# Kernel optimization log

Hardware: AMD Instinct MI355X
Metric: run time of the kernel (lower is better)

The kernel has to match this reference:

```python
import jax, jax.numpy as jnp
import numpy as np

N_HEADS = 32
N_KV_HEADS = 8
HEAD_DIM = 64
D_MODEL = 2048
SLIDING_WINDOW = 512
ROPE_THETA = 10000.0
PAST_LENGTH = 0
EPS = 1e-6


def setup_inputs() -> dict:
    key = jax.random.key(0)
    k1, k2, k3 = jax.random.split(key, 3)
    B, S = 1, 2048
    q_size = N_HEADS * HEAD_DIM
    kv_size = N_KV_HEADS * HEAD_DIM
    return {
        "x": jax.random.normal(k1, (B, S, D_MODEL), dtype=jnp.float32),
        "w_qkv": jax.random.normal(k2, (q_size + 2 * kv_size, D_MODEL), dtype=jnp.float32) * (D_MODEL ** -0.5),
        "w_out": jax.random.normal(k3, (D_MODEL, q_size), dtype=jnp.float32) * (q_size ** -0.5),
        "q_norm_w": jnp.ones((HEAD_DIM,), dtype=jnp.float32),
        "k_norm_w": jnp.ones((HEAD_DIM,), dtype=jnp.float32),
    }


def _rms_norm(x, w):
    xf = x.astype(jnp.float32)
    rms = jax.lax.rsqrt(jnp.mean(xf * xf, axis=-1, keepdims=True) + EPS)
    return (xf * rms).astype(x.dtype) * w


def _rope(q, k, past_length):
    # q: [b, h, s, d], k: [b, kv, s, d]
    s, d = q.shape[2], q.shape[3]
    inv_freq = 1.0 / (ROPE_THETA ** (jnp.arange(0, d, 2, dtype=jnp.float32) / d))
    pos = jnp.arange(s, dtype=jnp.float32) + past_length
    ang = pos[:, None] * inv_freq[None, :]            # [s, d/2]
    emb = jnp.concatenate([ang, ang], axis=-1)        # [s, d]
    cos, sin = jnp.cos(emb), jnp.sin(emb)

    def rot_half(x):
        x1, x2 = jnp.split(x, 2, axis=-1)
        return jnp.concatenate([-x2, x1], axis=-1)

    q = q * cos + rot_half(q) * sin
    k = k * cos + rot_half(k) * sin
    return q, k


def _sliding_mask(seq_len, total_len, past_length):
    q_idx = jnp.arange(seq_len)[:, None]
    k_idx = jnp.arange(total_len)[None, :]
    causal = (q_idx + past_length) >= k_idx
    window = (q_idx + past_length - k_idx) < SLIDING_WINDOW
    keep = causal & window
    return jnp.where(keep, 0.0, -jnp.inf).astype(jnp.float32)[None, None]


def reference(x, w_qkv, w_out, q_norm_w, k_norm_w):
    b, s, _ = x.shape
    n_rep = N_HEADS // N_KV_HEADS
    q_size = N_HEADS * HEAD_DIM
    kv_size = N_KV_HEADS * HEAD_DIM

    qkv = jnp.einsum('bsd,od->bso', x, w_qkv)
    q, k, v = jnp.split(qkv, [q_size, q_size + kv_size], axis=-1)
    q = q.reshape(b, s, N_HEADS, HEAD_DIM).transpose(0, 2, 1, 3)
    k = k.reshape(b, s, N_KV_HEADS, HEAD_DIM).transpose(0, 2, 1, 3)
    v = v.reshape(b, s, N_KV_HEADS, HEAD_DIM).transpose(0, 2, 1, 3)

    q = _rms_norm(q, q_norm_w)
    k = _rms_norm(k, k_norm_w)
    q, k = _rope(q, k, PAST_LENGTH)

    k_rep = jnp.repeat(k, n_rep, axis=1)  # [b, H, s, d]
    v_rep = jnp.repeat(v, n_rep, axis=1)

    scale = HEAD_DIM ** -0.5
    scores = jnp.einsum('bhqd,bhkd->bhqk', q, k_rep) * scale
    scores = scores + _sliding_mask(s, s, PAST_LENGTH)
    probs = jax.nn.softmax(scores, axis=-1)
    attn = jnp.einsum('bhqk,bhkd->bhqd', probs, v_rep)

    attn = attn.transpose(0, 2, 1, 3).reshape(b, s, q_size)
    return jnp.einsum('bso,do->bsd', attn, w_out)
```

## Files before the change

kernel.cpp:

```cpp
#include <hip/hip_runtime.h>

typedef unsigned short u16;
typedef unsigned int u32;
typedef __bf16 bf16x8 __attribute__((ext_vector_type(8)));
typedef float f32x4 __attribute__((ext_vector_type(4)));
typedef float f32x16 __attribute__((ext_vector_type(16)));
typedef u16 u16x8 __attribute__((ext_vector_type(8)));
typedef u32 u32x2 __attribute__((ext_vector_type(2)));
typedef u32 u32x4 __attribute__((ext_vector_type(4)));

#define MFMA16(a, b, c) __builtin_amdgcn_mfma_f32_16x16x32_bf16((a), (b), (c), 0, 0, 0)
#define MFMA32(a, b, c) __builtin_amdgcn_mfma_f32_32x32x16_bf16((a), (b), (c), 0, 0, 0)

__device__ __forceinline__ u16 f2bf(float f) {
    unsigned int u = __float_as_uint(f);
    u = (u + 0x7FFF + ((u >> 16) & 1)) >> 16;
    return (u16)u;
}

__device__ __forceinline__ u32 cvtpk(float a, float b) {
    u32 d;
    asm("v_cvt_pk_bf16_f32 %0, %1, %2" : "=v"(d) : "v"(a), "v"(b));
    return d;
}

__device__ __forceinline__ void gld_lds16(const u16* g, u16* l) {
    __builtin_amdgcn_global_load_lds(
        (const __attribute__((address_space(1))) unsigned int*)g,
        (__attribute__((address_space(3))) unsigned int*)l, 16, 0, 0);
}

__global__ __launch_bounds__(256) void cvt_bf16(const float* __restrict__ in,
                                                u16* __restrict__ out, int n4) {
    int idx = blockIdx.x * blockDim.x + threadIdx.x;
    int stride = gridDim.x * blockDim.x;
    for (int i = idx; i < n4; i += stride) {
        float4 v = reinterpret_cast<const float4*>(in)[i];
        ushort4 o;
        o.x = f2bf(v.x); o.y = f2bf(v.y); o.z = f2bf(v.z); o.w = f2bf(v.w);
        reinterpret_cast<ushort4*>(out)[i] = o;
    }
}

__global__ __launch_bounds__(256) void reduce_add(const float4* __restrict__ a,
                                                  const float4* __restrict__ b,
                                                  float4* __restrict__ o, int n4) {
    int idx = blockIdx.x * blockDim.x + threadIdx.x;
    int stride = gridDim.x * blockDim.x;
    for (int i = idx; i < n4; i += stride) {
        float4 va = a[i], vb = b[i];
        float4 vo = {va.x + vb.x, va.y + vb.y, va.z + vb.z, va.w + vb.w};
        o[i] = vo;
    }
}

template <int SPLITK>
__global__ __launch_bounds__(256) void gemm_bt(const u16* __restrict__ A,
                                               const u16* __restrict__ B,
                                               float* __restrict__ C,
                                               int M, int N, int K) {
    __shared__ __align__(16) u16 As[3][128 * 32];
    __shared__ __align__(16) u16 Bs[3][128 * 32];

    int nbn = N >> 7;
    int bid = blockIdx.x;
    int nwg = (M >> 7) * nbn;
    int cpx = nwg >> 3;
    int wg = (bid & 7) * cpx + (bid >> 3);
    int tm = wg / nbn, tn = wg % nbn;
    int m0 = tm << 7, n0 = tn << 7;

    int Ks = K / SPLITK;
    int kbase = blockIdx.y * Ks;
    float* Cs = C + (size_t)blockIdx.y * ((size_t)M * N);

    int t = threadIdx.x;
    int w = t >> 6, l = t & 63, lrow = l & 15, lhi = l >> 4;
    int wr = w >> 1, wc = w & 1;

    int e0 = t * 8;
    int row0 = t >> 2;
    int col0 = (((t & 3) ^ ((t >> 3) & 3)) << 3);

    const u16* Ag = A + (size_t)m0 * K + kbase;
    const u16* Bg = B + (size_t)n0 * K + kbase;

    auto stage = [&](int sbuf, int kt) {
        int k0 = kt << 5;
        gld_lds16(Ag + (size_t)row0 * K + k0 + col0, &As[sbuf][e0]);
        gld_lds16(Ag + (size_t)(row0 + 64) * K + k0 + col0, &As[sbuf][e0 + 2048]);
        gld_lds16(Bg + (size_t)row0 * K + k0 + col0, &Bs[sbuf][e0]);
        gld_lds16(Bg + (size_t)(row0 + 64) * K + k0 + col0, &Bs[sbuf][e0 + 2048]);
    };

    f32x4 acc[4][4] = {};
    int NT = Ks >> 5;
    stage(0, 0); stage(1, 1); stage(2, 2);
    asm volatile("s_waitcnt vmcnt(8)" ::: "memory");
    asm volatile("s_barrier" ::: "memory");
    int cur = 0;
    for (int kt = 0; kt < NT; ++kt) {
        bf16x8 af[4], bfr[4];
#pragma unroll
        for (int i = 0; i < 4; ++i) {
            int row = wr * 64 + i * 16 + lrow;
            af[i] = *(const bf16x8*)&As[cur][row * 32 + ((lhi ^ ((row >> 1) & 3)) << 3)];
        }
#pragma unroll
        for (int j = 0; j < 4; ++j) {
            int row = wc * 64 + j * 16 + lrow;
            bfr[j] = *(const bf16x8*)&Bs[cur][row * 32 + ((lhi ^ ((row >> 1) & 3)) << 3)];
        }
        asm volatile("s_waitcnt lgkmcnt(0)" ::: "memory");
        __builtin_amdgcn_sched_barrier(0);
        asm volatile("s_barrier" ::: "memory");
        if (kt + 3 < NT) stage(cur, kt + 3);
#pragma unroll
        for (int i = 0; i < 4; ++i)
#pragma unroll
            for (int j = 0; j < 4; ++j)
                acc[i][j] = MFMA16(af[i], bfr[j], acc[i][j]);
        if (kt + 1 < NT) {
            if (kt + 3 < NT)      asm volatile("s_waitcnt vmcnt(8)" ::: "memory");
            else if (kt + 2 < NT) asm volatile("s_waitcnt vmcnt(4)" ::: "memory");
            else                  asm volatile("s_waitcnt vmcnt(0)" ::: "memory");
            asm volatile("s_barrier" ::: "memory");
        }
        cur = (cur == 2) ? 0 : cur + 1;
    }
#pragma unroll
    for (int i = 0; i < 4; ++i) {
#pragma unroll
        for (int j = 0; j < 4; ++j) {
            int crow = m0 + wr * 64 + i * 16 + lhi * 4;
            int ccol = n0 + wc * 64 + j * 16 + lrow;
            float* cp = Cs + (size_t)crow * N + ccol;
#pragma unroll
            for (int r2 = 0; r2 < 4; ++r2) cp[(size_t)r2 * N] = acc[i][j][r2];
        }
    }
}

__global__ __launch_bounds__(256) void qkv_post(const float* __restrict__ qkv0,
                                                const float* __restrict__ qkv1,
                                                const float* __restrict__ qw,
                                                const float* __restrict__ kw,
                                                u16* __restrict__ qb,
                                                u16* __restrict__ kb,
                                                u16* __restrict__ vb) {
    const float C = 0.18033688011112042f;
    int s = blockIdx.x;
    int t = threadIdx.x, w = t >> 6, lane = t & 63;
    const float* row0 = qkv0 + (size_t)s * 3072;
    const float* row1 = qkv1 + (size_t)s * 3072;
    int d2 = lane & 31;
    float inv = exp2f(-(float)d2 * (13.287712379549449f / 32.0f));
    float ang = (float)s * inv;
    float cs = cosf(ang), sn = sinf(ang);
    for (int h = w; h < 48; h += 4) {
        float v = row0[h * 64 + lane] + row1[h * 64 + lane];
        if (h < 40) {
            float ss = v * v;
#pragma unroll
            for (int m = 32; m; m >>= 1) ss += __shfl_xor(ss, m);
            float rms = rsqrtf(ss * (1.0f / 64.0f) + 1e-6f);
            float wgt = (h < 32) ? qw[lane] : kw[lane];
            v = v * rms * wgt;
            float part = __shfl_xor(v, 32);
            float rot = (lane < 32) ? -part : part;
            v = v * cs + rot * sn;
            if (h < 32)
                qb[((size_t)h * 2048 + s) * 64 + lane] = f2bf(v * C);
            else
                kb[((size_t)(h - 32) * 2048 + s) * 64 + lane] = f2bf(v);
        } else {
            vb[((size_t)(h - 40) * 2048 + s) * 64 + lane] = f2bf(v);
        }
    }
}

__global__ __launch_bounds__(256) void transpose_v(const u16* __restrict__ vb,
                                                   u16* __restrict__ vt) {
    int kv = blockIdx.y;
    int s0 = blockIdx.x * 256;
    __shared__ __align__(16) u16 tile[64][256];
    int t = threadIdx.x;
    int sl = t >> 3;
    int d0 = (t & 7) * 8;
#pragma unroll
    for (int j = 0; j < 8; ++j) {
        int s = sl + j * 32;
        u16x8 v = *(const u16x8*)(vb + ((size_t)kv * 2048 + s0 + s) * 64 + d0);
#pragma unroll
        for (int e = 0; e < 8; ++e) tile[d0 + e][s] = v[e];
    }
    __syncthreads();
    int d = t >> 2;
    int so = (t & 3) * 64;
#pragma unroll
    for (int j = 0; j < 8; ++j) {
        int s_local = so + j * 8;
        *(u16x8*)(vt + ((size_t)kv * 64 + d) * 2048 + s0 + s_local) =
            *(const u16x8*)&tile[d][s_local];
    }
}

__global__ __launch_bounds__(256) void attn_fa7(const u16* __restrict__ qb,
                                                const u16* __restrict__ kb,
                                                const u16* __restrict__ vt,
                                                u16* __restrict__ ab) {
    int qt = blockIdx.x, h = blockIdx.y, kv = h >> 2;
    int t = threadIdx.x, w = t >> 6, l = t & 63;
    int lq = l & 31, hi = l >> 5;
    int qlo_blk = qt * 128;
    int qlo = qlo_blk + w * 32;
    __shared__ __align__(16) u16 Kt[2][32 * 64];
    __shared__ __align__(16) u16 Vt[2][64 * 32];
    __shared__ u16 sm[4][32][66];

    const u16* qrow = qb + ((size_t)h * 2048 + qlo + lq) * 64 + hi * 8;
    bf16x8 qf[4];
#pragma unroll
    for (int dk = 0; dk < 4; ++dk) qf[dk] = *(const bf16x8*)(qrow + dk * 16);

    f32x16 oa = {}, ob = {};
    float lsum = 0.f;

    int ktA = (qlo_blk >= 512) ? ((qlo_blk >> 5) - 16) : 0;
    int ktB = (qlo_blk >> 5) + 3;
    const u16* kb_h = kb + (size_t)kv * 2048 * 64;
    const u16* vt_h = vt + (size_t)kv * 64 * 2048;

    int sk_row = t >> 3, sk_c = ((t & 7) ^ (sk_row & 7)) << 3;
    int sv_row = t >> 2, sv_c = (((t & 3) ^ ((t >> 3) & 3))) << 3;

    auto stage = [&](int buf, int kt) {
        int k0 = kt << 5;
        gld_lds16(kb_h + (size_t)(k0 + sk_row) * 64 + sk_c, &Kt[buf][t * 8]);
        gld_lds16(vt_h + (size_t)sv_row * 2048 + k0 + sv_c, &Vt[buf][t * 8]);
    };

    stage(0, ktA);
    int cur = 0;
    for (int kt = ktA; kt <= ktB; ++kt) {
        if (kt < ktB) {
            stage(cur ^ 1, kt + 1);
            asm volatile("s_waitcnt vmcnt(2)" ::: "memory");
        } else {
            asm volatile("s_waitcnt vmcnt(0)" ::: "memory");
        }
        asm volatile("s_barrier" ::: "memory");

        int k0 = kt << 5;
        bool active = (k0 <= qlo + 31) && (k0 >= qlo - 542);
        if (active) {
            bf16x8 kf[4], vaf[2], vbf[2];
#pragma unroll
            for (int c = 0; c < 4; ++c)
                kf[c] = *(const bf16x8*)&Kt[cur][lq * 64 + (((c * 2 + hi) ^ (lq & 7)) << 3)];
#pragma unroll
            for (int vi = 0; vi < 2; ++vi) {
                int swz = ((vi * 2 + hi) ^ ((lq >> 1) & 3)) << 3;
                vaf[vi] = *(const bf16x8*)&Vt[cur][lq * 32 + swz];
                vbf[vi] = *(const bf16x8*)&Vt[cur][(lq + 32) * 32 + swz];
            }
            asm volatile("s_waitcnt lgkmcnt(0)" ::: "memory");
            __builtin_amdgcn_sched_barrier(0);

            f32x16 s = {};
            s = MFMA32(kf[0], qf[0], s);
            s = MFMA32(kf[1], qf[1], s);
            s = MFMA32(kf[2], qf[2], s);
            s = MFMA32(kf[3], qf[3], s);

            bool edge = (k0 + 31 > qlo) || (qlo + 31 - k0 >= 512);
            if (edge) {
                int q = qlo + lq;
#pragma unroll
                for (int r = 0; r < 16; ++r) {
                    int k = k0 + (r & 3) + 8 * (r >> 2) + 4 * hi;
                    if (!((unsigned)(q - k) < 512u)) s[r] = -1e30f;
                }
            }
            float p[16];
#pragma unroll
            for (int r = 0; r < 16; ++r) {
                p[r] = exp2f(s[r]);
                lsum += p[r];
            }
            u32 pk0 = cvtpk(p[0], p[1]),   pk1 = cvtpk(p[2], p[3]);
            u32 pk2 = cvtpk(p[4], p[5]),   pk3 = cvtpk(p[6], p[7]);
            u32 pk4 = cvtpk(p[8], p[9]),   pk5 = cvtpk(p[10], p[11]);
            u32 pk6 = cvtpk(p[12], p[13]), pk7 = cvtpk(p[14], p[15]);
            u32x2 r02 = __builtin_amdgcn_permlane32_swap(pk0, pk2, false, false);
            u32x2 r13 = __builtin_amdgcn_permlane32_swap(pk1, pk3, false, false);
            u32x2 r46 = __builtin_amdgcn_permlane32_swap(pk4, pk6, false, false);
            u32x2 r57 = __builtin_amdgcn_permlane32_swap(pk5, pk7, false, false);
            bf16x8 b0, b1;
            {
                u32* bp = (u32*)&b0;
                bp[0] = r02[0]; bp[1] = r13[0]; bp[2] = r02[1]; bp[3] = r13[1];
                u32* bq = (u32*)&b1;
                bq[0] = r46[0]; bq[1] = r57[0]; bq[2] = r46[1]; bq[3] = r57[1];
            }
            oa = MFMA32(vaf[0], b0, oa);
            oa = MFMA32(vaf[1], b1, oa);
            ob = MFMA32(vbf[0], b0, ob);
            ob = MFMA32(vbf[1], b1, ob);
        }
        asm volatile("s_barrier" ::: "memory");
        cur ^= 1;
    }

    lsum += __shfl_xor(lsum, 32);
    float inv = 1.0f / lsum;
#pragma unroll
    for (int rp = 0; rp < 8; ++rp) {
        int r = rp * 2;
        int d = (r & 3) + 8 * (r >> 2) + 4 * hi;
        *(u32*)&sm[w][lq][d]      = cvtpk(oa[r] * inv, oa[r + 1] * inv);
        *(u32*)&sm[w][lq][d + 32] = cvtpk(ob[r] * inv, ob[r + 1] * inv);
    }
    asm volatile("s_waitcnt lgkmcnt(0)" ::: "memory");
    int qr = l >> 1, dbase = (l & 1) * 32;
    size_t orow = (size_t)(qlo + qr) * 2048 + h * 64 + dbase;
#pragma unroll
    for (int c2 = 0; c2 < 8; ++c2) {
        u32 w0 = *(const u32*)&sm[w][qr][dbase + c2 * 4];
        u32 w1 = *(const u32*)&sm[w][qr][dbase + c2 * 4 + 2];
        u32x2 val = { w0, w1 };
        *(u32x2*)(ab + orow + c2 * 4) = val;
    }
}

extern "C" void kernel_launch(void* const* d_in, const int* in_sizes, int n_in,
                              void* d_out, int out_size, void* d_ws, size_t ws_size,
                              hipStream_t stream) {
    const float* x     = (const float*)d_in[0];
    const float* w_qkv = (const float*)d_in[1];
    const float* w_out = (const float*)d_in[2];
    const float* qw    = (const float*)d_in[3];
    const float* kw    = (const float*)d_in[4];
    float* out = (float*)d_out;

    char* ws = (char*)d_ws;
    u16*   x_b    = (u16*)(ws);
    u16*   wB     = (u16*)(ws + 8388608);
    u16*   q_b    = (u16*)(ws);
    u16*   k_b    = (u16*)(ws + 8388608);
    u16*   v_b    = (u16*)(ws + 10485760);
    u16*   v_t    = (u16*)(ws + 12582912);
    float* P0     = (float*)(ws + 20971520);
    float* O0     = (float*)(ws + 20971520);
    float* O1     = (float*)(ws + 37748736);
    u16*   attn_b = (u16*)(ws + 54525952);

    cvt_bf16<<<2048, 256, 0, stream>>>(x, x_b, 2048 * 2048 / 4);
    cvt_bf16<<<2048, 256, 0, stream>>>(w_qkv, wB, 3072 * 2048 / 4);
    gemm_bt<2><<<dim3(384, 2), 256, 0, stream>>>(x_b, wB, P0, 2048, 3072, 2048);
    qkv_post<<<2048, 256, 0, stream>>>(P0, P0 + (size_t)2048 * 3072, qw, kw, q_b, k_b, v_b);
    transpose_v<<<dim3(8, 8), 256, 0, stream>>>(v_b, v_t);
    attn_fa7<<<dim3(16, 32), 256, 0, stream>>>(q_b, k_b, v_t, attn_b);
    cvt_bf16<<<2048, 256, 0, stream>>>(w_out, wB, 2048 * 2048 / 4);
    gemm_bt<2><<<dim3(256, 2), 256, 0, stream>>>(attn_b, wB, O0, 2048, 2048, 2048);
    reduce_add<<<1024, 256, 0, stream>>>((const float4*)O0, (const float4*)O1,
                                         (float4*)out, 2048 * 2048 / 4);
}
```

Before: 142.4 us.

## Give each wave private LDS tiles in gemm_bt to remove block barriers

Each wave now stages its own 64-row A slice and 64-row B slice into a private LDS region, so the gemm's triple-buffered pipeline no longer needs workgroup-wide s_barrier synchronization, only per-wave vmcnt waits. This removes barrier stalls between waves. The cost is that data shared between waves (A rows shared by waves with the same wr, B rows by the same wc) is now loaded twice from global memory. LDS use also doubles, from 48KB to 96KB per block, which may reduce occupancy.

```diff
diff --git a/kernel.cpp b/kernel.cpp
--- a/kernel.cpp
+++ b/kernel.cpp
@@ -59,8 +59,7 @@
                                                const u16* __restrict__ B,
                                                float* __restrict__ C,
                                                int M, int N, int K) {
-    __shared__ __align__(16) u16 As[3][128 * 32];
-    __shared__ __align__(16) u16 Bs[3][128 * 32];
+    __shared__ __align__(16) u16 lds[4][3][4096];
 
     int nbn = N >> 7;
     int bid = blockIdx.x;
@@ -78,54 +77,54 @@
     int w = t >> 6, l = t & 63, lrow = l & 15, lhi = l >> 4;
     int wr = w >> 1, wc = w & 1;
 
-    int e0 = t * 8;
-    int row0 = t >> 2;
-    int col0 = (((t & 3) ^ ((t >> 3) & 3)) << 3);
-
-    const u16* Ag = A + (size_t)m0 * K + kbase;
-    const u16* Bg = B + (size_t)n0 * K + kbase;
-
-    auto stage = [&](int sbuf, int kt) {
+    int srow = l >> 2;
+    int scol = (((l & 3) ^ ((l >> 3) & 3)) << 3);
+
+    const u16* Ag = A + (size_t)(m0 + wr * 64) * K + kbase;
+    const u16* Bg = B + (size_t)(n0 + wc * 64) * K + kbase;
+
+    auto stage = [&](int b, int kt) {
         int k0 = kt << 5;
-        gld_lds16(Ag + (size_t)row0 * K + k0 + col0, &As[sbuf][e0]);
-        gld_lds16(Ag + (size_t)(row0 + 64) * K + k0 + col0, &As[sbuf][e0 + 2048]);
-        gld_lds16(Bg + (size_t)row0 * K + k0 + col0, &Bs[sbuf][e0]);
-        gld_lds16(Bg + (size_t)(row0 + 64) * K + k0 + col0, &Bs[sbuf][e0 + 2048]);
+        u16* dst = &lds[w][b][0];
+#pragma unroll
+        for (int n = 0; n < 4; ++n)
+            gld_lds16(Ag + (size_t)(n * 16 + srow) * K + k0 + scol,
+                      dst + n * 512 + l * 8);
+#pragma unroll
+        for (int n = 0; n < 4; ++n)
+            gld_lds16(Bg + (size_t)(n * 16 + srow) * K + k0 + scol,
+                      dst + 2048 + n * 512 + l * 8);
     };
 
     f32x4 acc[4][4] = {};
     int NT = Ks >> 5;
     stage(0, 0); stage(1, 1); stage(2, 2);
-    asm volatile("s_waitcnt vmcnt(8)" ::: "memory");
-    asm volatile("s_barrier" ::: "memory");
+    asm volatile("s_waitcnt vmcnt(16)" ::: "memory");
+    __builtin_amdgcn_sched_barrier(0);
+
     int cur = 0;
     for (int kt = 0; kt < NT; ++kt) {
+        const u16* base = &lds[w][cur][0];
         bf16x8 af[4], bfr[4];
 #pragma unroll
         for (int i = 0; i < 4; ++i) {
-            int row = wr * 64 + i * 16 + lrow;
-            af[i] = *(const bf16x8*)&As[cur][row * 32 + ((lhi ^ ((row >> 1) & 3)) << 3)];
-        }
-#pragma unroll
-        for (int j = 0; j < 4; ++j) {
-            int row = wc * 64 + j * 16 + lrow;
-            bfr[j] = *(const bf16x8*)&Bs[cur][row * 32 + ((lhi ^ ((row >> 1) & 3)) << 3)];
+            int row = i * 16 + lrow;
+            int swz = (lhi ^ ((lrow >> 1) & 3)) << 3;
+            af[i]  = *(const bf16x8*)(base + row * 32 + swz);
+            bfr[i] = *(const bf16x8*)(base + 2048 + row * 32 + swz);
         }
         asm volatile("s_waitcnt lgkmcnt(0)" ::: "memory");
         __builtin_amdgcn_sched_barrier(0);
-        asm volatile("s_barrier" ::: "memory");
         if (kt + 3 < NT) stage(cur, kt + 3);
 #pragma unroll
         for (int i = 0; i < 4; ++i)
 #pragma unroll
             for (int j = 0; j < 4; ++j)
                 acc[i][j] = MFMA16(af[i], bfr[j], acc[i][j]);
-        if (kt + 1 < NT) {
-            if (kt + 3 < NT)      asm volatile("s_waitcnt vmcnt(8)" ::: "memory");
-            else if (kt + 2 < NT) asm volatile("s_waitcnt vmcnt(4)" ::: "memory");
-            else                  asm volatile("s_waitcnt vmcnt(0)" ::: "memory");
-            asm volatile("s_barrier" ::: "memory");
-        }
+        if (kt + 3 < NT)      asm volatile("s_waitcnt vmcnt(16)" ::: "memory");
+        else if (kt + 2 < NT) asm volatile("s_waitcnt vmcnt(8)"  ::: "memory");
+        else if (kt + 1 < NT) asm volatile("s_waitcnt vmcnt(0)"  ::: "memory");
+        __builtin_amdgcn_sched_barrier(0);
         cur = (cur == 2) ? 0 : cur + 1;
     }
 #pragma unroll
```

After: 158.2 us. 11.1% more time.
